# Kernel tuning notes

Measured on AMD Instinct MI355X. Metric: run time of the kernel, lower is better.

Reference implementation:

```python
import jax, jax.numpy as jnp
import numpy as np

N, E, IN_DIM, HID, HEADS, LAYERS, NUM_STORES = 50000, 800000, 64, 128, 16, 3, 50
DH = HID // HEADS  # per-head dim = 8
EPS = 1e-5


def setup_inputs() -> dict:
    key = jax.random.key(0)
    ks = iter(jax.random.split(key, 40))
    def nrm(shape, scale):
        return jax.random.normal(next(ks), shape, dtype=jnp.float32) * scale
    inp = {}
    inp['x'] = jax.random.normal(next(ks), (N, IN_DIM), dtype=jnp.float32)
    inp['edge_index'] = jax.random.randint(next(ks), (2, E), 0, N, dtype=jnp.int32)
    inp['edge_weight'] = jax.random.uniform(next(ks), (E, 1), dtype=jnp.float32)
    inp['store_mask'] = jax.random.randint(next(ks), (N,), 0, NUM_STORES, dtype=jnp.int32)
    # input_proj: Linear + GELU + LayerNorm
    inp['in_W'] = nrm((IN_DIM, HID), IN_DIM ** -0.5)
    inp['in_b'] = jnp.zeros((HID,), jnp.float32)
    inp['in_g'] = jnp.ones((HID,), jnp.float32)
    inp['in_beta'] = jnp.zeros((HID,), jnp.float32)
    # 3 stacked GATv2 layers (stacked leading dim = layer)
    s = HID ** -0.5
    inp['gat_Wl'] = nrm((LAYERS, HID, HID), s)
    inp['gat_bl'] = jnp.zeros((LAYERS, HID), jnp.float32)
    inp['gat_Wr'] = nrm((LAYERS, HID, HID), s)
    inp['gat_br'] = jnp.zeros((LAYERS, HID), jnp.float32)
    inp['gat_We'] = nrm((LAYERS, 1, HID), 1.0)
    inp['gat_att'] = nrm((LAYERS, HEADS, DH), DH ** -0.5)
    inp['gat_bias'] = jnp.zeros((LAYERS, HID), jnp.float32)
    inp['blk_g'] = jnp.ones((LAYERS, HID), jnp.float32)
    inp['blk_b'] = jnp.zeros((LAYERS, HID), jnp.float32)
    # per-store context gate + final norm
    inp['ctx_W'] = nrm((HID, HID), s)
    inp['ctx_b'] = jnp.zeros((HID,), jnp.float32)
    inp['fin_g'] = jnp.ones((HID,), jnp.float32)
    inp['fin_b'] = jnp.zeros((HID,), jnp.float32)
    return inp


def layernorm(x, g, b):
    mu = jnp.mean(x, axis=-1, keepdims=True)
    v = jnp.mean((x - mu) ** 2, axis=-1, keepdims=True)
    return (x - mu) * jax.lax.rsqrt(v + EPS) * g + b


def gatv2_layer(x, src, dst, ea, Wl, bl, Wr, br, We, att, bias):
    # x: [N, HID]; src/dst: [Et]; ea: [Et, 1]
    n = x.shape[0]
    xl = (x @ Wl + bl).reshape(n, HEADS, DH)   # source transform
    xr = (x @ Wr + br).reshape(n, HEADS, DH)   # target transform
    ee = (ea @ We).reshape(-1, HEADS, DH)      # edge-attr embedding
    e = jax.nn.leaky_relu(xl[src] + xr[dst] + ee, 0.2)  # [Et, H, D]
    logit = jnp.einsum('ehd,hd->eh', e, att)             # [Et, H]
    # segment softmax over incoming edges of each target node
    mx = jax.ops.segment_max(logit, dst, num_segments=n)
    p = jnp.exp(logit - mx[dst])
    Z = jax.ops.segment_sum(p, dst, num_segments=n)
    alpha = p / (Z[dst] + 1e-16)
    msg = alpha[:, :, None] * xl[src]                    # [Et, H, D]
    agg = jax.ops.segment_sum(msg, dst, num_segments=n)  # [N, H, D]
    return agg.reshape(n, HEADS * DH) + bias


def forward(x, edge_index, edge_weight, store_mask, in_W, in_b, in_g, in_beta,
            gat_Wl, gat_bl, gat_Wr, gat_br, gat_We, gat_att, gat_bias,
            blk_g, blk_b, ctx_W, ctx_b, fin_g, fin_b):
    n = x.shape[0]
    h = layernorm(jax.nn.gelu(x @ in_W + in_b, approximate=False), in_g, in_beta)
    src, dst = edge_index[0], edge_index[1]
    # PyG add_self_loops with fill_value='mean': per-target mean of incoming edge attrs
    deg = jax.ops.segment_sum(jnp.ones(src.shape, h.dtype), dst, num_segments=n)
    loop_attr = jax.ops.segment_sum(edge_weight, dst, num_segments=n) / jnp.maximum(deg, 1.0)[:, None]
    loops = jnp.arange(n, dtype=src.dtype)
    srcf = jnp.concatenate([src, loops])
    dstf = jnp.concatenate([dst, loops])
    eaf = jnp.concatenate([edge_weight, loop_attr], axis=0)
    for l in range(LAYERS):  # residual block: post-norm residual around conv
        m = gatv2_layer(h, srcf, dstf, eaf, gat_Wl[l], gat_bl[l], gat_Wr[l], gat_br[l],
                        gat_We[l], gat_att[l], gat_bias[l])
        h = layernorm(h + m, blk_g[l], blk_b[l])
    # per-store segmented mean -> sigmoid gate -> scatter back
    cnt = jax.ops.segment_sum(jnp.ones((n,), h.dtype), store_mask, num_segments=NUM_STORES)
    means = jax.ops.segment_sum(h, store_mask, num_segments=NUM_STORES) / jnp.maximum(cnt, 1.0)[:, None]
    gate = jax.nn.sigmoid(means @ ctx_W + ctx_b)
    h = h + (gate * means)[store_mask]
    return layernorm(h, fin_g, fin_b)


def reference(x, edge_index, edge_weight, store_mask, in_W, in_b, in_g, in_beta,
              gat_Wl, gat_bl, gat_Wr, gat_br, gat_We, gat_att, gat_bias,
              blk_g, blk_b, ctx_W, ctx_b, fin_g, fin_b):
    return forward(x, edge_index, edge_weight, store_mask, in_W, in_b, in_g, in_beta,
                   gat_Wl, gat_bl, gat_Wr, gat_br, gat_We, gat_att, gat_bias,
                   blk_g, blk_b, ctx_W, ctx_b, fin_g, fin_b)
```

## Files before the change

kernel.cpp:

```cpp
#include <hip/hip_runtime.h>
#include <math.h>

#define NN 50000
#define EE 800000
#define ET (EE + NN)
#define HID 128
#define NSTORE 50
#define NBL 196
#define CNT_B 3125
#define XCV_B 3125
#define WCV_B 192
#define IWC_B 32
#define SCT_B 3321
#define GEMB 391
#define SSB 512
#define ATT_B 2048

typedef unsigned short ushort_t;
typedef unsigned long long u64;
typedef __attribute__((ext_vector_type(8))) short bf8;
typedef __attribute__((ext_vector_type(4))) float f4;
typedef __attribute__((ext_vector_type(2))) float f2;
typedef __attribute__((ext_vector_type(4))) unsigned int u4;

__device__ __forceinline__ ushort_t f2b(float f) {
    union { float f; unsigned int i; } v; v.f = f;
    unsigned int r = (v.i + 0x7fffu + ((v.i >> 16) & 1u)) >> 16;
    return (ushort_t)r;
}
__device__ __forceinline__ f2 b2f2v(unsigned int u) {
    union { unsigned int i; float f; } lo, hi;
    lo.i = u << 16; hi.i = u & 0xffff0000u;
    f2 r; r.x = lo.f; r.y = hi.f; return r;
}
__device__ __forceinline__ unsigned int pk2(float lo, float hi) {
    return (unsigned int)f2b(lo) | ((unsigned int)f2b(hi) << 16);
}
__device__ __forceinline__ f2 max2(f2 a, f2 b) {
#if __has_builtin(__builtin_elementwise_max)
    return __builtin_elementwise_max(a, b);
#else
    f2 r; r.x = fmaxf(a.x, b.x); r.y = fmaxf(a.y, b.y); return r;
#endif
}

__global__ __launch_bounds__(256) void k_build(const int* __restrict__ ei, const float* __restrict__ ew,
                                               const float* __restrict__ x, const float* __restrict__ inW,
                                               const float* __restrict__ gWl, const float* __restrict__ gWr,
                                               ushort_t* __restrict__ xb, ushort_t* __restrict__ inWt,
                                               ushort_t* __restrict__ Wlt, ushort_t* __restrict__ Wrt,
                                               u64* __restrict__ packed, int* __restrict__ rank) {
    int b = blockIdx.x, t = threadIdx.x;
    if (b < CNT_B) {
        int i = b * 256 + t;
        int dst = ei[EE + i];
        unsigned int wfix = __float2uint_rn(ew[i] * 16777216.0f);
        u64 old = atomicAdd(&packed[dst], (1ULL << 44) | (u64)wfix);
        rank[i] = (int)(old >> 44);
        return;
    }
    if (b < CNT_B + XCV_B) {
        int i = ((b - CNT_B) * 256 + t) * 4;
        f4 v = *(const f4*)(x + i);
        uint2 p; p.x = pk2(v.x, v.y); p.y = pk2(v.z, v.w);
        *(uint2*)(xb + i) = p;
        return;
    }
    if (b < CNT_B + XCV_B + WCV_B) {
        int i = (b - CNT_B - XCV_B) * 256 + t;
        int l = i >> 14, r = i & 16383, nn2 = r >> 7, k = r & 127;
        Wlt[i] = f2b(gWl[(size_t)l * 16384 + k * 128 + nn2]);
        Wrt[i] = f2b(gWr[(size_t)l * 16384 + k * 128 + nn2]);
        return;
    }
    {
        int i = (b - CNT_B - XCV_B - WCV_B) * 256 + t;
        int c = i >> 6, k = i & 63;
        inWt[i] = f2b(inW[k * 128 + c]);
    }
}

__global__ __launch_bounds__(256) void k_inproj(const ushort_t* __restrict__ A,
                                                const ushort_t* __restrict__ Wt,
                                                const float* __restrict__ bias,
                                                const float* __restrict__ g,
                                                const float* __restrict__ be,
                                                ushort_t* __restrict__ hb) {
    const int K = 64;
    __shared__ float s1[2][128], s2[2][128];
    int lane = threadIdx.x & 63, w = threadIdx.x >> 6;
    int rw = w >> 1, cw = w & 1;
    int q = lane >> 4, l16 = lane & 15;
    int row0 = blockIdx.x * 128 + rw * 64;
    int col0 = cw * 64;
    bf8 z; for (int t = 0; t < 8; ++t) z[t] = 0;

    bf8 bfr[2][4];
#pragma unroll
    for (int kk = 0; kk < 2; ++kk)
#pragma unroll
        for (int j = 0; j < 4; ++j)
            bfr[kk][j] = *(const bf8*)(Wt + (size_t)(col0 + j * 16 + l16) * K + kk * 32 + q * 8);

    f4 acc[4][4];
#pragma unroll
    for (int i = 0; i < 4; ++i)
#pragma unroll
        for (int j = 0; j < 4; ++j) acc[i][j] = (f4)(0.f);

#pragma unroll
    for (int kk = 0; kk < 2; ++kk) {
        bf8 af[4];
#pragma unroll
        for (int i = 0; i < 4; ++i) {
            int r = row0 + i * 16 + l16;
            af[i] = (r < NN) ? *(const bf8*)(A + (size_t)r * K + kk * 32 + q * 8) : z;
        }
#pragma unroll
        for (int i = 0; i < 4; ++i)
#pragma unroll
            for (int j = 0; j < 4; ++j)
                acc[i][j] = __builtin_amdgcn_mfma_f32_16x16x32_bf16(af[i], bfr[kk][j], acc[i][j], 0, 0, 0);
    }
#pragma unroll
    for (int i = 0; i < 4; ++i) {
#pragma unroll
        for (int j = 0; j < 4; ++j) {
            float bv = bias[col0 + j * 16 + l16];
#pragma unroll
            for (int r = 0; r < 4; ++r) {
                float v = acc[i][j][r] + bv;
                v = 0.5f * v * (1.f + erff(v * 0.70710678118654752f));
                acc[i][j][r] = v;
            }
        }
    }
#pragma unroll
    for (int i = 0; i < 4; ++i) {
#pragma unroll
        for (int r = 0; r < 4; ++r) {
            float sm = acc[i][0][r] + acc[i][1][r] + acc[i][2][r] + acc[i][3][r];
            float sq = acc[i][0][r] * acc[i][0][r] + acc[i][1][r] * acc[i][1][r]
                     + acc[i][2][r] * acc[i][2][r] + acc[i][3][r] * acc[i][3][r];
#pragma unroll
            for (int k = 1; k < 16; k <<= 1) { sm += __shfl_xor(sm, k); sq += __shfl_xor(sq, k); }
            if (l16 == 0) {
                int rl = rw * 64 + i * 16 + q * 4 + r;
                s1[cw][rl] = sm; s2[cw][rl] = sq;
            }
        }
    }
    __syncthreads();
#pragma unroll
    for (int i = 0; i < 4; ++i) {
#pragma unroll
        for (int r = 0; r < 4; ++r) {
            int rl = rw * 64 + i * 16 + q * 4 + r;
            int gr = blockIdx.x * 128 + rl;
            if (gr >= NN) continue;
            float sm = s1[0][rl] + s1[1][rl];
            float sq = s2[0][rl] + s2[1][rl];
            float mu = sm * (1.f / 128.f);
            float var = sq * (1.f / 128.f) - mu * mu;
            float rinv = rsqrtf(var + 1e-5f);
#pragma unroll
            for (int j = 0; j < 4; ++j) {
                int gc = col0 + j * 16 + l16;
                float v = (acc[i][j][r] - mu) * rinv * g[gc] + be[gc];
                hb[(size_t)gr * HID + gc] = f2b(v);
            }
        }
    }
}

__global__ __launch_bounds__(256) void k_psum(const u64* __restrict__ packed, int* __restrict__ bsum) {
    int t = threadIdx.x, bidx = blockIdx.x;
    int i = bidx * 256 + t;
    int v = (i < NN) ? (int)(packed[i] >> 44) + 1 : 0;
#pragma unroll
    for (int d = 1; d < 64; d <<= 1) v += __shfl_xor(v, d);
    __shared__ int ws4[4];
    if ((t & 63) == 0) ws4[t >> 6] = v;
    __syncthreads();
    if (t == 0) bsum[bidx] = ws4[0] + ws4[1] + ws4[2] + ws4[3];
}

__global__ __launch_bounds__(256) void k_scanb(const int* __restrict__ bsum,
                                               int* __restrict__ bbase, int* __restrict__ offs) {
    __shared__ int s[256];
    int t = threadIdx.x;
    int v = (t < NBL) ? bsum[t] : 0;
    s[t] = v;
    __syncthreads();
    for (int d = 1; d < 256; d <<= 1) {
        int u = (t >= d) ? s[t - d] : 0;
        __syncthreads();
        s[t] += u;
        __syncthreads();
    }
    if (t < NBL) bbase[t] = s[t] - v;
    if (t == 0) offs[NN] = ET;
}

__global__ __launch_bounds__(256) void k_offs(const u64* __restrict__ packed,
                                              const int* __restrict__ bbase, int* __restrict__ offs) {
    __shared__ int wsum4[4];
    int t = threadIdx.x, bidx = blockIdx.x;
    int i = bidx * 256 + t;
    int v = (i < NN) ? (int)(packed[i] >> 44) + 1 : 0;
    int lane = t & 63, w = t >> 6;
    int sc = v;
#pragma unroll
    for (int d = 1; d < 64; d <<= 1) {
        int u = __shfl_up(sc, d);
        if (lane >= d) sc += u;
    }
    if (lane == 63) wsum4[w] = sc;
    __syncthreads();
    int wo = 0;
    for (int k = 0; k < w; ++k) wo += wsum4[k];
    if (i < NN) offs[i] = bbase[bidx] + wo + sc - v;
}

__global__ __launch_bounds__(256) void k_gemm2(const ushort_t* __restrict__ A,
                                               const ushort_t* __restrict__ Wt0,
                                               const ushort_t* __restrict__ Wt1,
                                               const float* __restrict__ b0,
                                               const float* __restrict__ b1,
                                               ushort_t* __restrict__ o0,
                                               ushort_t* __restrict__ o1, int n,
                                               const int* __restrict__ ei,
                                               const float* __restrict__ ew,
                                               const int* __restrict__ offs,
                                               const u64* __restrict__ packed,
                                               const int* __restrict__ rank,
                                               int2* __restrict__ csr) {
    int bid = blockIdx.x;
    if (bid >= 2 * GEMB) {
        int i = (bid - 2 * GEMB) * 256 + threadIdx.x;
        if (i < EE) {
            int src = ei[i], dst = ei[EE + i];
            int pos = offs[dst] + rank[i];
            int2 v; v.x = src << 8; v.y = __float_as_int(ew[i]);
            csr[pos] = v;
        } else if (i < ET) {
            int nd = i - EE;
            u64 p = packed[nd];
            int deg = (int)(p >> 44);
            float wsf = (float)(p & ((1ULL << 44) - 1)) * (1.0f / 16777216.0f);
            float la = wsf / fmaxf((float)deg, 1.0f);
            int pos = offs[nd + 1] - 1;
            int2 v; v.x = nd << 8; v.y = __float_as_int(la);
            csr[pos] = v;
        }
        return;
    }
    const int K = 128;
    int by = (bid >= GEMB) ? 1 : 0;
    int bx = by ? bid - GEMB : bid;
    const ushort_t* Wt = by ? Wt1 : Wt0;
    const float* bias = by ? b1 : b0;
    ushort_t* outb = by ? o1 : o0;
    int lane = threadIdx.x & 63, w = threadIdx.x >> 6;
    int rw = w >> 1, cw = w & 1;
    int q = lane >> 4, l16 = lane & 15;
    int row0 = bx * 128 + rw * 64;
    int col0 = cw * 64;
    bf8 z; for (int t = 0; t < 8; ++t) z[t] = 0;

    bf8 bfr[4][4];
#pragma unroll
    for (int kk = 0; kk < 4; ++kk)
#pragma unroll
        for (int j = 0; j < 4; ++j)
            bfr[kk][j] = *(const bf8*)(Wt + (size_t)(col0 + j * 16 + l16) * K + kk * 32 + q * 8);

    f4 acc[4][4];
#pragma unroll
    for (int i = 0; i < 4; ++i)
#pragma unroll
        for (int j = 0; j < 4; ++j) acc[i][j] = (f4)(0.f);

#pragma unroll
    for (int kk = 0; kk < 4; ++kk) {
        bf8 af[4];
#pragma unroll
        for (int i = 0; i < 4; ++i) {
            int r = row0 + i * 16 + l16;
            af[i] = (r < n) ? *(const bf8*)(A + (size_t)r * K + kk * 32 + q * 8) : z;
        }
#pragma unroll
        for (int i = 0; i < 4; ++i)
#pragma unroll
            for (int j = 0; j < 4; ++j)
                acc[i][j] = __builtin_amdgcn_mfma_f32_16x16x32_bf16(af[i], bfr[kk][j], acc[i][j], 0, 0, 0);
    }
#pragma unroll
    for (int i = 0; i < 4; ++i) {
        int gr0 = row0 + i * 16 + q * 4;
#pragma unroll
        for (int j = 0; j < 4; ++j) {
            int gc = col0 + j * 16 + l16;
            float bv = bias[gc];
#pragma unroll
            for (int r = 0; r < 4; ++r) {
                int gr = gr0 + r;
                if (gr < n) outb[(size_t)gr * HID + gc] = f2b(acc[i][j][r] + bv);
            }
        }
    }
}

__global__ __launch_bounds__(256, 4) void k_attn(const ushort_t* __restrict__ xl,
                                                 const ushort_t* __restrict__ xr,
                                                 ushort_t* __restrict__ hb,
                                                 const int* __restrict__ offs,
                                                 const int2* __restrict__ csr,
                                                 const float* __restrict__ We,
                                                 const float* __restrict__ att,
                                                 const float* __restrict__ gbias,
                                                 const float* __restrict__ g,
                                                 const float* __restrict__ b) {
    int lane = threadIdx.x & 63;
    int wslot = threadIdx.x >> 6;
    int hd = lane & 15;
    int grp = lane >> 4;
    int dbase = hd * 8;
    int db2 = hd * 16;

    f2 at2[4], we2[4];
    {
        f4 a0 = *(const f4*)(att + dbase), a1 = *(const f4*)(att + dbase + 4);
        at2[0].x = a0.x; at2[0].y = a0.y; at2[1].x = a0.z; at2[1].y = a0.w;
        at2[2].x = a1.x; at2[2].y = a1.y; at2[3].x = a1.z; at2[3].y = a1.w;
        f4 w0 = *(const f4*)(We + dbase), w1 = *(const f4*)(We + dbase + 4);
        we2[0].x = w0.x; we2[0].y = w0.y; we2[1].x = w0.z; we2[1].y = w0.w;
        we2[2].x = w1.x; we2[2].y = w1.y; we2[3].x = w1.z; we2[3].y = w1.w;
    }

    for (int wid = blockIdx.x * 4 + wslot; wid < NN; wid += ATT_B * 4) {
        size_t base = (size_t)wid * HID;
        f2 xr2[4];
        {
            u4 uxr = *(const u4*)(xr + base + dbase);
            xr2[0] = b2f2v(uxr.x); xr2[1] = b2f2v(uxr.y);
            xr2[2] = b2f2v(uxr.z); xr2[3] = b2f2v(uxr.w);
        }
        int p0 = offs[wid], p1 = offs[wid + 1];
        int deg = p1 - p0;
        int nmain = deg > 64 ? 64 : deg;
        int2 rec = csr[p0 + ((lane < deg) ? lane : deg - 1)];

        float Z = 0.f;
        f2 acc2[4];
#pragma unroll
        for (int q = 0; q < 4; ++q) { acc2[q].x = 0.f; acc2[q].y = 0.f; }

#define ISSUE(K, UX, EA)                                                       \
    {                                                                          \
        int ie_ = e0 + 4 * K + grp;                                            \
        int is_ = (ie_ < nmain) ? ie_ : 0;                                     \
        EA = __int_as_float(__shfl(rec.y, is_));                               \
        int sx_ = __shfl(rec.x, is_);                                          \
        UX = *(const u4*)((const char*)xl + (unsigned)sx_ + db2);              \
    }

#define COMP(K, UX, EA)                                                        \
    {                                                                          \
        bool vm_ = (e0 + 4 * K + grp) < nmain;                                 \
        f2 x2_[4];                                                             \
        x2_[0] = b2f2v(UX.x); x2_[1] = b2f2v(UX.y);                            \
        x2_[2] = b2f2v(UX.z); x2_[3] = b2f2v(UX.w);                            \
        f2 lg2_; lg2_.x = 0.f; lg2_.y = 0.f;                                   \
        _Pragma("unroll")                                                      \
        for (int q_ = 0; q_ < 4; ++q_) {                                       \
            f2 t_ = (x2_[q_] + xr2[q_]) + EA * we2[q_];                        \
            t_ = max2(t_, t_ * 0.2f);                                          \
            lg2_ += at2[q_] * t_;                                              \
        }                                                                      \
        float w_ = vm_ ? __expf(lg2_.x + lg2_.y) : 0.f;                        \
        Z += w_;                                                               \
        _Pragma("unroll")                                                      \
        for (int q_ = 0; q_ < 4; ++q_) acc2[q_] += w_ * x2_[q_];               \
    }

        for (int e0 = 0; e0 < nmain; e0 += 16) {
            u4 uxA, uxB, uxC, uxD;
            float eaA, eaB, eaC, eaD;
            ISSUE(0, uxA, eaA)
            ISSUE(1, uxB, eaB)
            ISSUE(2, uxC, eaC)
            ISSUE(3, uxD, eaD)
            COMP(0, uxA, eaA)
            COMP(1, uxB, eaB)
            COMP(2, uxC, eaC)
            COMP(3, uxD, eaD)
        }
#undef ISSUE
#undef COMP

        for (int e = p0 + 64; e < p1; e += 4) {
            int ei_ = e + grp;
            bool vm_ = ei_ < p1;
            int2 m2_ = csr[vm_ ? ei_ : p1 - 1];
            float ea_ = __int_as_float(m2_.y);
            u4 ux_ = *(const u4*)((const char*)xl + (unsigned)m2_.x + db2);
            f2 x2_[4];
            x2_[0] = b2f2v(ux_.x); x2_[1] = b2f2v(ux_.y);
            x2_[2] = b2f2v(ux_.z); x2_[3] = b2f2v(ux_.w);
            f2 lg2_; lg2_.x = 0.f; lg2_.y = 0.f;
#pragma unroll
            for (int q_ = 0; q_ < 4; ++q_) {
                f2 t_ = (x2_[q_] + xr2[q_]) + ea_ * we2[q_];
                t_ = max2(t_, t_ * 0.2f);
                lg2_ += at2[q_] * t_;
            }
            float w_ = vm_ ? __expf(lg2_.x + lg2_.y) : 0.f;
            Z += w_;
#pragma unroll
            for (int q_ = 0; q_ < 4; ++q_) acc2[q_] += w_ * x2_[q_];
        }

        Z += __shfl_xor(Z, 16); Z += __shfl_xor(Z, 32);
#pragma unroll
        for (int q = 0; q < 4; ++q) {
            acc2[q].x += __shfl_xor(acc2[q].x, 16);
            acc2[q].x += __shfl_xor(acc2[q].x, 32);
            acc2[q].y += __shfl_xor(acc2[q].y, 16);
            acc2[q].y += __shfl_xor(acc2[q].y, 32);
        }
        float inv = 1.f / (Z + 1e-16f);
        float acc[8] = {acc2[0].x, acc2[0].y, acc2[1].x, acc2[1].y,
                        acc2[2].x, acc2[2].y, acc2[3].x, acc2[3].y};

        u4 uh = *(const u4*)(hb + base + dbase);
        f2 hr0 = b2f2v(uh.x), hr1 = b2f2v(uh.y), hr2 = b2f2v(uh.z), hr3 = b2f2v(uh.w);
        float hres[8] = {hr0.x, hr0.y, hr1.x, hr1.y, hr2.x, hr2.y, hr3.x, hr3.y};
        f4 gb0 = *(const f4*)(gbias + dbase), gb1 = *(const f4*)(gbias + dbase + 4);
        float gb8[8] = {gb0.x, gb0.y, gb0.z, gb0.w, gb1.x, gb1.y, gb1.z, gb1.w};
        float o[8], sm = 0.f, sq = 0.f;
#pragma unroll
        for (int q = 0; q < 8; ++q) {
            o[q] = acc[q] * inv + gb8[q] + hres[q];
            sm += o[q]; sq += o[q] * o[q];
        }
#pragma unroll
        for (int k = 1; k < 16; k <<= 1) { sm += __shfl_xor(sm, k); sq += __shfl_xor(sq, k); }
        float mu = sm * (1.f / 128.f);
        float var = sq * (1.f / 128.f) - mu * mu;
        float rinv = rsqrtf(var + 1e-5f);
        f4 g0 = *(const f4*)(g + dbase), g1 = *(const f4*)(g + dbase + 4);
        float g8[8] = {g0.x, g0.y, g0.z, g0.w, g1.x, g1.y, g1.z, g1.w};
        f4 b0 = *(const f4*)(b + dbase), b1 = *(const f4*)(b + dbase + 4);
        float b8[8] = {b0.x, b0.y, b0.z, b0.w, b1.x, b1.y, b1.z, b1.w};
        float v8[8];
#pragma unroll
        for (int q = 0; q < 8; ++q) v8[q] = (o[q] - mu) * rinv * g8[q] + b8[q];
        if (grp == 0) {
            u4 hu;
            hu.x = pk2(v8[0], v8[1]); hu.y = pk2(v8[2], v8[3]);
            hu.z = pk2(v8[4], v8[5]); hu.w = pk2(v8[6], v8[7]);
            *(u4*)(hb + base + dbase) = hu;
        }
    }
}

__global__ __launch_bounds__(256) void k_store_sum(const ushort_t* __restrict__ hb,
                                                   const int* __restrict__ mask,
                                                   float* __restrict__ psums,
                                                   int* __restrict__ pcnts) {
    __shared__ float ls[NSTORE * HID];
    __shared__ int lc[NSTORE];
    int t = threadIdx.x, bidx = blockIdx.x;
    for (int i = t; i < NSTORE * HID; i += 256) ls[i] = 0.f;
    if (t < NSTORE) lc[t] = 0;
    __syncthreads();
    int wid = bidx * 4 + (t >> 6);
    int lane = t & 63;
    int nw = SSB * 4;
    int d0 = lane * 2;
    for (int node = wid; node < NN; node += nw) {
        int s = mask[node];
        unsigned int hv = ((const unsigned int*)(hb + (size_t)node * HID))[lane];
        f2 v = b2f2v(hv);
        atomicAdd(&ls[s * HID + d0], v.x);
        atomicAdd(&ls[s * HID + d0 + 1], v.y);
        if (lane == 0) atomicAdd(&lc[s], 1);
    }
    __syncthreads();
    for (int i = t; i < NSTORE * HID; i += 256) psums[(size_t)bidx * (NSTORE * HID) + i] = ls[i];
    if (t < NSTORE) pcnts[bidx * NSTORE + t] = lc[t];
}

__global__ __launch_bounds__(256) void k_gate(const float* __restrict__ psums,
                                              const int* __restrict__ pcnts,
                                              const float* __restrict__ ctxW,
                                              const float* __restrict__ ctxb,
                                              float* __restrict__ gm) {
    __shared__ float h1[HID];
    __shared__ float mloc[HID];
    __shared__ int cw4[4];
    int s = blockIdx.x, t = threadIdx.x;
    int d = t & 127, half = t >> 7;
    float s0 = 0.f, s1 = 0.f, s2 = 0.f, s3 = 0.f;
    for (int b = half * 4; b < SSB; b += 8) {
        s0 += psums[(size_t)(b + 0) * (NSTORE * HID) + s * HID + d];
        s1 += psums[(size_t)(b + 1) * (NSTORE * HID) + s * HID + d];
        s2 += psums[(size_t)(b + 2) * (NSTORE * HID) + s * HID + d];
        s3 += psums[(size_t)(b + 3) * (NSTORE * HID) + s * HID + d];
    }
    float sum = (s0 + s1) + (s2 + s3);
    int c = pcnts[t * NSTORE + s] + pcnts[(t + 256) * NSTORE + s];
#pragma unroll
    for (int k = 1; k < 64; k <<= 1) c += __shfl_xor(c, k);
    if ((t & 63) == 0) cw4[t >> 6] = c;
    if (half) h1[d] = sum;
    __syncthreads();
    if (half == 0) {
        float tot = sum + h1[d];
        float cnt = fmaxf((float)(cw4[0] + cw4[1] + cw4[2] + cw4[3]), 1.f);
        mloc[d] = tot / cnt;
    }
    __syncthreads();
    if (half == 0) {
        float acc = ctxb[d];
        for (int j = 0; j < HID; ++j) acc += mloc[j] * ctxW[j * HID + d];
        float gate = 1.f / (1.f + __expf(-acc));
        gm[s * HID + d] = gate * mloc[d];
    }
}

__global__ __launch_bounds__(256) void k_final(const ushort_t* __restrict__ hb,
                                               const int* __restrict__ mask,
                                               const float* __restrict__ gm,
                                               const float* __restrict__ g,
                                               const float* __restrict__ b,
                                               float* __restrict__ out) {
    int wid = (blockIdx.x * 256 + threadIdx.x) >> 6;
    int lane = threadIdx.x & 63;
    if (wid >= NN) return;
    size_t base = (size_t)wid * HID;
    int s = mask[wid];
    int d0 = lane * 2, d1 = d0 + 1;
    unsigned int hv = ((const unsigned int*)(hb + base))[lane];
    f2 hvv = b2f2v(hv);
    float v0 = hvv.x + gm[s * HID + d0];
    float v1 = hvv.y + gm[s * HID + d1];
    float sm = v0 + v1, sq = v0 * v0 + v1 * v1;
#pragma unroll
    for (int k = 1; k < 64; k <<= 1) { sm += __shfl_xor(sm, k); sq += __shfl_xor(sq, k); }
    float mu = sm * (1.f / 128.f);
    float var = sq * (1.f / 128.f) - mu * mu;
    float r = rsqrtf(var + 1e-5f);
    out[base + d0] = (v0 - mu) * r * g[d0] + b[d0];
    out[base + d1] = (v1 - mu) * r * g[d1] + b[d1];
}

extern "C" void kernel_launch(void* const* d_in, const int* in_sizes, int n_in,
                              void* d_out, int out_size, void* d_ws, size_t ws_size,
                              hipStream_t stream) {
    const float* x      = (const float*)d_in[0];
    const int*   ei     = (const int*)d_in[1];
    const float* ew     = (const float*)d_in[2];
    const int*   smask  = (const int*)d_in[3];
    const float* inW    = (const float*)d_in[4];
    const float* inb    = (const float*)d_in[5];
    const float* ing    = (const float*)d_in[6];
    const float* inbeta = (const float*)d_in[7];
    const float* gWl    = (const float*)d_in[8];
    const float* gbl    = (const float*)d_in[9];
    const float* gWr    = (const float*)d_in[10];
    const float* gbr    = (const float*)d_in[11];
    const float* gWe    = (const float*)d_in[12];
    const float* gatt   = (const float*)d_in[13];
    const float* gbias  = (const float*)d_in[14];
    const float* blkg   = (const float*)d_in[15];
    const float* blkb   = (const float*)d_in[16];
    const float* ctxW   = (const float*)d_in[17];
    const float* ctxb   = (const float*)d_in[18];
    const float* fing   = (const float*)d_in[19];
    const float* finb   = (const float*)d_in[20];
    float* out = (float*)d_out;

    float* ws = (float*)d_ws;
    size_t o = 0;
    int2*     csr    = (int2*)(ws + o);     o += (size_t)ET * 2;
    float*    gm     = ws + o;              o += NSTORE * HID;
    int*      offs   = (int*)(ws + o);      o += 50004;
    int*      rank   = (int*)(ws + o);      o += EE;
    ushort_t* xb     = (ushort_t*)(ws + o); o += (size_t)NN * 64 / 2;
    ushort_t* hb     = (ushort_t*)(ws + o); o += (size_t)NN * HID / 2;
    ushort_t* xlb    = (ushort_t*)(ws + o); o += (size_t)NN * HID / 2;
    ushort_t* xrb    = (ushort_t*)(ws + o); o += (size_t)NN * HID / 2;
    ushort_t* inWt   = (ushort_t*)(ws + o); o += 128 * 64 / 2;
    ushort_t* Wlt    = (ushort_t*)(ws + o); o += 3 * 128 * 128 / 2;
    ushort_t* Wrt    = (ushort_t*)(ws + o); o += 3 * 128 * 128 / 2;
    int*      bsum   = (int*)(ws + o);      o += 256;
    int*      bbase  = (int*)(ws + o);      o += 256;
    float*    psums  = ws + o;              o += (size_t)SSB * NSTORE * HID;
    int*      pcnts  = (int*)(ws + o);      o += SSB * NSTORE;
    if (o & 1) ++o;
    float*    zbase  = ws + o;
    u64*      packed = (u64*)(ws + o);      o += (size_t)NN * 2;
    size_t zbytes = (size_t)(NN * 2) * 4;

    hipMemsetAsync((void*)zbase, 0, zbytes, stream);

    const int WB = NN / 4;

    k_build<<<CNT_B + XCV_B + WCV_B + IWC_B, 256, 0, stream>>>(ei, ew, x, inW, gWl, gWr,
                                                               xb, inWt, Wlt, Wrt, packed, rank);
    k_inproj<<<GEMB, 256, 0, stream>>>(xb, inWt, inb, ing, inbeta, hb);
    k_psum<<<NBL, 256, 0, stream>>>(packed, bsum);
    k_scanb<<<1, 256, 0, stream>>>(bsum, bbase, offs);
    k_offs<<<NBL, 256, 0, stream>>>(packed, bbase, offs);

    for (int l = 0; l < 3; ++l) {
        int nb = 2 * GEMB + (l == 0 ? SCT_B : 0);
        k_gemm2<<<nb, 256, 0, stream>>>(hb, Wlt + (size_t)l * HID * HID, Wrt + (size_t)l * HID * HID,
                                        gbl + l * HID, gbr + l * HID, xlb, xrb, NN,
                                        ei, ew, offs, packed, rank, csr);
        k_attn<<<ATT_B, 256, 0, stream>>>(xlb, xrb, hb, offs, csr,
                                          gWe + l * HID, gatt + l * HID, gbias + l * HID,
                                          blkg + l * HID, blkb + l * HID);
    }

    k_store_sum<<<SSB, 256, 0, stream>>>(hb, smask, psums, pcnts);
    k_gate<<<NSTORE, 256, 0, stream>>>(psums, pcnts, ctxW, ctxb, gm);
    k_final<<<WB, 256, 0, stream>>>(hb, smask, gm, fing, finb, out);
}
```

Measured before the change: 532.1 us.

## Launch one wave per node in attention and split full/tail edge loops

The attention kernel now runs one wave per destination node with a grid of NN/4 blocks, replacing the persistent grid-stride loop, and drops the occupancy hint from launch bounds. The edge loop is split into full 16-edge chunks that skip per-edge validity masks and a masked 4-edge tail. Node offsets are also precomputed as (start, end) int2 pairs so each wave reads its range in one load. This trades launch and scheduling overhead for removing loop-carried state, and the changed register budget could alter occupancy.

```diff
diff --git a/kernel.cpp b/kernel.cpp
--- a/kernel.cpp
+++ b/kernel.cpp
@@ -14,7 +14,6 @@
 #define SCT_B 3321
 #define GEMB 391
 #define SSB 512
-#define ATT_B 2048
 
 typedef unsigned short ushort_t;
 typedef unsigned long long u64;
@@ -203,7 +202,8 @@
 }
 
 __global__ __launch_bounds__(256) void k_offs(const u64* __restrict__ packed,
-                                              const int* __restrict__ bbase, int* __restrict__ offs) {
+                                              const int* __restrict__ bbase, int* __restrict__ offs,
+                                              int2* __restrict__ oprs) {
     __shared__ int wsum4[4];
     int t = threadIdx.x, bidx = blockIdx.x;
     int i = bidx * 256 + t;
@@ -219,7 +219,12 @@
     __syncthreads();
     int wo = 0;
     for (int k = 0; k < w; ++k) wo += wsum4[k];
-    if (i < NN) offs[i] = bbase[bidx] + wo + sc - v;
+    if (i < NN) {
+        int p0 = bbase[bidx] + wo + sc - v;
+        offs[i] = p0;
+        int2 pr; pr.x = p0; pr.y = p0 + v;
+        oprs[i] = pr;
+    }
 }
 
 __global__ __launch_bounds__(256) void k_gemm2(const ushort_t* __restrict__ A,
@@ -311,25 +316,36 @@
     }
 }
 
-__global__ __launch_bounds__(256, 4) void k_attn(const ushort_t* __restrict__ xl,
-                                                 const ushort_t* __restrict__ xr,
-                                                 ushort_t* __restrict__ hb,
-                                                 const int* __restrict__ offs,
-                                                 const int2* __restrict__ csr,
-                                                 const float* __restrict__ We,
-                                                 const float* __restrict__ att,
-                                                 const float* __restrict__ gbias,
-                                                 const float* __restrict__ g,
-                                                 const float* __restrict__ b) {
+__global__ __launch_bounds__(256) void k_attn(const ushort_t* __restrict__ xl,
+                                              const ushort_t* __restrict__ xr,
+                                              ushort_t* __restrict__ hb,
+                                              const int2* __restrict__ oprs,
+                                              const int2* __restrict__ csr,
+                                              const float* __restrict__ We,
+                                              const float* __restrict__ att,
+                                              const float* __restrict__ gbias,
+                                              const float* __restrict__ g,
+                                              const float* __restrict__ b) {
+    int wid = (blockIdx.x * 256 + threadIdx.x) >> 6;
     int lane = threadIdx.x & 63;
-    int wslot = threadIdx.x >> 6;
+    if (wid >= NN) return;
     int hd = lane & 15;
     int grp = lane >> 4;
     int dbase = hd * 8;
     int db2 = hd * 16;
-
-    f2 at2[4], we2[4];
+    size_t base = (size_t)wid * HID;
+
+    int2 pr = oprs[wid];
+    int p0 = pr.x, p1 = pr.y;
+    int deg = p1 - p0;
+    int nmain = deg > 64 ? 64 : deg;
+    int2 rec = csr[p0 + ((lane < deg) ? lane : deg - 1)];
+
+    f2 xr2[4], at2[4], we2[4];
     {
+        u4 uxr = *(const u4*)(xr + base + dbase);
+        xr2[0] = b2f2v(uxr.x); xr2[1] = b2f2v(uxr.y);
+        xr2[2] = b2f2v(uxr.z); xr2[3] = b2f2v(uxr.w);
         f4 a0 = *(const f4*)(att + dbase), a1 = *(const f4*)(att + dbase + 4);
         at2[0].x = a0.x; at2[0].y = a0.y; at2[1].x = a0.z; at2[1].y = a0.w;
         at2[2].x = a1.x; at2[2].y = a1.y; at2[3].x = a1.z; at2[3].y = a1.w;
@@ -338,36 +354,20 @@
         we2[2].x = w1.x; we2[2].y = w1.y; we2[3].x = w1.z; we2[3].y = w1.w;
     }
 
-    for (int wid = blockIdx.x * 4 + wslot; wid < NN; wid += ATT_B * 4) {
-        size_t base = (size_t)wid * HID;
-        f2 xr2[4];
-        {
-            u4 uxr = *(const u4*)(xr + base + dbase);
-            xr2[0] = b2f2v(uxr.x); xr2[1] = b2f2v(uxr.y);
-            xr2[2] = b2f2v(uxr.z); xr2[3] = b2f2v(uxr.w);
-        }
-        int p0 = offs[wid], p1 = offs[wid + 1];
-        int deg = p1 - p0;
-        int nmain = deg > 64 ? 64 : deg;
-        int2 rec = csr[p0 + ((lane < deg) ? lane : deg - 1)];
-
-        float Z = 0.f;
-        f2 acc2[4];
-#pragma unroll
-        for (int q = 0; q < 4; ++q) { acc2[q].x = 0.f; acc2[q].y = 0.f; }
-
-#define ISSUE(K, UX, EA)                                                       \
+    float Z = 0.f;
+    f2 acc2[4];
+#pragma unroll
+    for (int q = 0; q < 4; ++q) { acc2[q].x = 0.f; acc2[q].y = 0.f; }
+
+#define ISSUEF(K, UX, EA)                                                      \
     {                                                                          \
-        int ie_ = e0 + 4 * K + grp;                                            \
-        int is_ = (ie_ < nmain) ? ie_ : 0;                                     \
+        int is_ = e0 + 4 * K + grp;                                            \
         EA = __int_as_float(__shfl(rec.y, is_));                               \
         int sx_ = __shfl(rec.x, is_);                                          \
         UX = *(const u4*)((const char*)xl + (unsigned)sx_ + db2);              \
     }
-
-#define COMP(K, UX, EA)                                                        \
+#define COMPF(UX, EA)                                                          \
     {                                                                          \
-        bool vm_ = (e0 + 4 * K + grp) < nmain;                                 \
         f2 x2_[4];                                                             \
         x2_[0] = b2f2v(UX.x); x2_[1] = b2f2v(UX.y);                            \
         x2_[2] = b2f2v(UX.z); x2_[3] = b2f2v(UX.w);                            \
@@ -378,90 +378,113 @@
             t_ = max2(t_, t_ * 0.2f);                                          \
             lg2_ += at2[q_] * t_;                                              \
         }                                                                      \
-        float w_ = vm_ ? __expf(lg2_.x + lg2_.y) : 0.f;                        \
+        float w_ = __expf(lg2_.x + lg2_.y);                                    \
         Z += w_;                                                               \
         _Pragma("unroll")                                                      \
         for (int q_ = 0; q_ < 4; ++q_) acc2[q_] += w_ * x2_[q_];               \
     }
 
-        for (int e0 = 0; e0 < nmain; e0 += 16) {
-            u4 uxA, uxB, uxC, uxD;
-            float eaA, eaB, eaC, eaD;
-            ISSUE(0, uxA, eaA)
-            ISSUE(1, uxB, eaB)
-            ISSUE(2, uxC, eaC)
-            ISSUE(3, uxD, eaD)
-            COMP(0, uxA, eaA)
-            COMP(1, uxB, eaB)
-            COMP(2, uxC, eaC)
-            COMP(3, uxD, eaD)
-        }
-#undef ISSUE
-#undef COMP
-
-        for (int e = p0 + 64; e < p1; e += 4) {
-            int ei_ = e + grp;
-            bool vm_ = ei_ < p1;
-            int2 m2_ = csr[vm_ ? ei_ : p1 - 1];
-            float ea_ = __int_as_float(m2_.y);
-            u4 ux_ = *(const u4*)((const char*)xl + (unsigned)m2_.x + db2);
-            f2 x2_[4];
-            x2_[0] = b2f2v(ux_.x); x2_[1] = b2f2v(ux_.y);
-            x2_[2] = b2f2v(ux_.z); x2_[3] = b2f2v(ux_.w);
-            f2 lg2_; lg2_.x = 0.f; lg2_.y = 0.f;
-#pragma unroll
-            for (int q_ = 0; q_ < 4; ++q_) {
-                f2 t_ = (x2_[q_] + xr2[q_]) + ea_ * we2[q_];
-                t_ = max2(t_, t_ * 0.2f);
-                lg2_ += at2[q_] * t_;
-            }
-            float w_ = vm_ ? __expf(lg2_.x + lg2_.y) : 0.f;
-            Z += w_;
-#pragma unroll
-            for (int q_ = 0; q_ < 4; ++q_) acc2[q_] += w_ * x2_[q_];
-        }
-
-        Z += __shfl_xor(Z, 16); Z += __shfl_xor(Z, 32);
-#pragma unroll
-        for (int q = 0; q < 4; ++q) {
-            acc2[q].x += __shfl_xor(acc2[q].x, 16);
-            acc2[q].x += __shfl_xor(acc2[q].x, 32);
-            acc2[q].y += __shfl_xor(acc2[q].y, 16);
-            acc2[q].y += __shfl_xor(acc2[q].y, 32);
-        }
-        float inv = 1.f / (Z + 1e-16f);
-        float acc[8] = {acc2[0].x, acc2[0].y, acc2[1].x, acc2[1].y,
-                        acc2[2].x, acc2[2].y, acc2[3].x, acc2[3].y};
-
-        u4 uh = *(const u4*)(hb + base + dbase);
-        f2 hr0 = b2f2v(uh.x), hr1 = b2f2v(uh.y), hr2 = b2f2v(uh.z), hr3 = b2f2v(uh.w);
-        float hres[8] = {hr0.x, hr0.y, hr1.x, hr1.y, hr2.x, hr2.y, hr3.x, hr3.y};
-        f4 gb0 = *(const f4*)(gbias + dbase), gb1 = *(const f4*)(gbias + dbase + 4);
-        float gb8[8] = {gb0.x, gb0.y, gb0.z, gb0.w, gb1.x, gb1.y, gb1.z, gb1.w};
-        float o[8], sm = 0.f, sq = 0.f;
-#pragma unroll
-        for (int q = 0; q < 8; ++q) {
-            o[q] = acc[q] * inv + gb8[q] + hres[q];
-            sm += o[q]; sq += o[q] * o[q];
-        }
-#pragma unroll
-        for (int k = 1; k < 16; k <<= 1) { sm += __shfl_xor(sm, k); sq += __shfl_xor(sq, k); }
-        float mu = sm * (1.f / 128.f);
-        float var = sq * (1.f / 128.f) - mu * mu;
-        float rinv = rsqrtf(var + 1e-5f);
-        f4 g0 = *(const f4*)(g + dbase), g1 = *(const f4*)(g + dbase + 4);
-        float g8[8] = {g0.x, g0.y, g0.z, g0.w, g1.x, g1.y, g1.z, g1.w};
-        f4 b0 = *(const f4*)(b + dbase), b1 = *(const f4*)(b + dbase + 4);
-        float b8[8] = {b0.x, b0.y, b0.z, b0.w, b1.x, b1.y, b1.z, b1.w};
-        float v8[8];
-#pragma unroll
-        for (int q = 0; q < 8; ++q) v8[q] = (o[q] - mu) * rinv * g8[q] + b8[q];
-        if (grp == 0) {
-            u4 hu;
-            hu.x = pk2(v8[0], v8[1]); hu.y = pk2(v8[2], v8[3]);
-            hu.z = pk2(v8[4], v8[5]); hu.w = pk2(v8[6], v8[7]);
-            *(u4*)(hb + base + dbase) = hu;
-        }
+    int nfull = nmain & ~15;
+    for (int e0 = 0; e0 < nfull; e0 += 16) {
+        u4 uxA, uxB, uxC, uxD;
+        float eaA, eaB, eaC, eaD;
+        ISSUEF(0, uxA, eaA)
+        ISSUEF(1, uxB, eaB)
+        ISSUEF(2, uxC, eaC)
+        ISSUEF(3, uxD, eaD)
+        COMPF(uxA, eaA)
+        COMPF(uxB, eaB)
+        COMPF(uxC, eaC)
+        COMPF(uxD, eaD)
+    }
+#undef ISSUEF
+#undef COMPF
+
+    for (int e0 = nfull; e0 < nmain; e0 += 4) {
+        int ie_ = e0 + grp;
+        bool vm_ = ie_ < nmain;
+        int is_ = vm_ ? ie_ : 0;
+        float ea_ = __int_as_float(__shfl(rec.y, is_));
+        int sx_ = __shfl(rec.x, is_);
+        u4 ux_ = *(const u4*)((const char*)xl + (unsigned)sx_ + db2);
+        f2 x2_[4];
+        x2_[0] = b2f2v(ux_.x); x2_[1] = b2f2v(ux_.y);
+        x2_[2] = b2f2v(ux_.z); x2_[3] = b2f2v(ux_.w);
+        f2 lg2_; lg2_.x = 0.f; lg2_.y = 0.f;
+#pragma unroll
+        for (int q_ = 0; q_ < 4; ++q_) {
+            f2 t_ = (x2_[q_] + xr2[q_]) + ea_ * we2[q_];
+            t_ = max2(t_, t_ * 0.2f);
+            lg2_ += at2[q_] * t_;
+        }
+        float w_ = vm_ ? __expf(lg2_.x + lg2_.y) : 0.f;
+        Z += w_;
+#pragma unroll
+        for (int q_ = 0; q_ < 4; ++q_) acc2[q_] += w_ * x2_[q_];
+    }
+
+    for (int e = p0 + 64; e < p1; e += 4) {
+        int ei_ = e + grp;
+        bool vm_ = ei_ < p1;
+        int2 m2_ = csr[vm_ ? ei_ : p1 - 1];
+        float ea_ = __int_as_float(m2_.y);
+        u4 ux_ = *(const u4*)((const char*)xl + (unsigned)m2_.x + db2);
+        f2 x2_[4];
+        x2_[0] = b2f2v(ux_.x); x2_[1] = b2f2v(ux_.y);
+        x2_[2] = b2f2v(ux_.z); x2_[3] = b2f2v(ux_.w);
+        f2 lg2_; lg2_.x = 0.f; lg2_.y = 0.f;
+#pragma unroll
+        for (int q_ = 0; q_ < 4; ++q_) {
+            f2 t_ = (x2_[q_] + xr2[q_]) + ea_ * we2[q_];
+            t_ = max2(t_, t_ * 0.2f);
+            lg2_ += at2[q_] * t_;
+        }
+        float w_ = vm_ ? __expf(lg2_.x + lg2_.y) : 0.f;
+        Z += w_;
+#pragma unroll
+        for (int q_ = 0; q_ < 4; ++q_) acc2[q_] += w_ * x2_[q_];
+    }
+
+    Z += __shfl_xor(Z, 16); Z += __shfl_xor(Z, 32);
+#pragma unroll
+    for (int q = 0; q < 4; ++q) {
+        acc2[q].x += __shfl_xor(acc2[q].x, 16);
+        acc2[q].x += __shfl_xor(acc2[q].x, 32);
+        acc2[q].y += __shfl_xor(acc2[q].y, 16);
+        acc2[q].y += __shfl_xor(acc2[q].y, 32);
+    }
+    float inv = 1.f / (Z + 1e-16f);
+    float acc[8] = {acc2[0].x, acc2[0].y, acc2[1].x, acc2[1].y,
+                    acc2[2].x, acc2[2].y, acc2[3].x, acc2[3].y};
+
+    u4 uh = *(const u4*)(hb + base + dbase);
+    f2 hr0 = b2f2v(uh.x), hr1 = b2f2v(uh.y), hr2 = b2f2v(uh.z), hr3 = b2f2v(uh.w);
+    float hres[8] = {hr0.x, hr0.y, hr1.x, hr1.y, hr2.x, hr2.y, hr3.x, hr3.y};
+    f4 gb0 = *(const f4*)(gbias + dbase), gb1 = *(const f4*)(gbias + dbase + 4);
+    float gb8[8] = {gb0.x, gb0.y, gb0.z, gb0.w, gb1.x, gb1.y, gb1.z, gb1.w};
+    float o[8], sm = 0.f, sq = 0.f;
+#pragma unroll
+    for (int q = 0; q < 8; ++q) {
+        o[q] = acc[q] * inv + gb8[q] + hres[q];
+        sm += o[q]; sq += o[q] * o[q];
+    }
+#pragma unroll
+    for (int k = 1; k < 16; k <<= 1) { sm += __shfl_xor(sm, k); sq += __shfl_xor(sq, k); }
+    float mu = sm * (1.f / 128.f);
+    float var = sq * (1.f / 128.f) - mu * mu;
+    float rinv = rsqrtf(var + 1e-5f);
+    f4 g0 = *(const f4*)(g + dbase), g1 = *(const f4*)(g + dbase + 4);
+    float g8[8] = {g0.x, g0.y, g0.z, g0.w, g1.x, g1.y, g1.z, g1.w};
+    f4 b0 = *(const f4*)(b + dbase), b1 = *(const f4*)(b + dbase + 4);
+    float b8[8] = {b0.x, b0.y, b0.z, b0.w, b1.x, b1.y, b1.z, b1.w};
+    float v8[8];
+#pragma unroll
+    for (int q = 0; q < 8; ++q) v8[q] = (o[q] - mu) * rinv * g8[q] + b8[q];
+    if (grp == 0) {
+        u4 hu;
+        hu.x = pk2(v8[0], v8[1]); hu.y = pk2(v8[2], v8[3]);
+        hu.z = pk2(v8[4], v8[5]); hu.w = pk2(v8[6], v8[7]);
+        *(u4*)(hb + base + dbase) = hu;
     }
 }
 
@@ -587,6 +610,7 @@
     int2*     csr    = (int2*)(ws + o);     o += (size_t)ET * 2;
     float*    gm     = ws + o;              o += NSTORE * HID;
     int*      offs   = (int*)(ws + o);      o += 50004;
+    int2*     oprs   = (int2*)(ws + o);     o += (size_t)NN * 2;
     int*      rank   = (int*)(ws + o);      o += EE;
     ushort_t* xb     = (ushort_t*)(ws + o); o += (size_t)NN * 64 / 2;
     ushort_t* hb     = (ushort_t*)(ws + o); o += (size_t)NN * HID / 2;
@@ -613,16 +637,16 @@
     k_inproj<<<GEMB, 256, 0, stream>>>(xb, inWt, inb, ing, inbeta, hb);
     k_psum<<<NBL, 256, 0, stream>>>(packed, bsum);
     k_scanb<<<1, 256, 0, stream>>>(bsum, bbase, offs);
-    k_offs<<<NBL, 256, 0, stream>>>(packed, bbase, offs);
+    k_offs<<<NBL, 256, 0, stream>>>(packed, bbase, offs, oprs);
 
     for (int l = 0; l < 3; ++l) {
         int nb = 2 * GEMB + (l == 0 ? SCT_B : 0);
         k_gemm2<<<nb, 256, 0, stream>>>(hb, Wlt + (size_t)l * HID * HID, Wrt + (size_t)l * HID * HID,
                                         gbl + l * HID, gbr + l * HID, xlb, xrb, NN,
                                         ei, ew, offs, packed, rank, csr);
-        k_attn<<<ATT_B, 256, 0, stream>>>(xlb, xrb, hb, offs, csr,
-                                          gWe + l * HID, gatt + l * HID, gbias + l * HID,
-                                          blkg + l * HID, blkb + l * HID);
+        k_attn<<<WB, 256, 0, stream>>>(xlb, xrb, hb, oprs, csr,
+                                       gWe + l * HID, gatt + l * HID, gbias + l * HID,
+                                       blkg + l * HID, blkb + l * HID);
     }
 
     k_store_sum<<<SSB, 256, 0, stream>>>(hb, smask, psums, pcnts);
```

Measured after the change: 522.2 us. No clear change (-1.9%).
